# Optimization experiments

Hardware: AMD Instinct MI355X
Metric: run time of the kernel (lower is better)

The kernel has to match this reference:

```python
import jax, jax.numpy as jnp
import numpy as np

NEG_SLOPE = 0.2


def gat_layer(x, W, a_src, a_dst, b, src, dst, num_nodes, heads, out_c, concat):
    # Linear transform per head: [N, heads, out_c]
    h = (x @ W).reshape(num_nodes, heads, out_c)
    # Per-node attention logits for source/dest roles: [N, heads]
    e_src = jnp.einsum('nhc,hc->nh', h, a_src)
    e_dst = jnp.einsum('nhc,hc->nh', h, a_dst)
    # Edge-wise scores (gather), LeakyReLU: [E, heads]
    e = jax.nn.leaky_relu(e_src[src] + e_dst[dst], negative_slope=NEG_SLOPE)
    # Segment softmax over incoming edges of each destination node
    m = jax.ops.segment_max(e, dst, num_segments=num_nodes)
    ex = jnp.exp(e - m[dst])
    denom = jax.ops.segment_sum(ex, dst, num_segments=num_nodes)
    alpha = ex / denom[dst]                       # [E, heads]
    # Weighted scatter-aggregate of source messages: [N, heads, out_c]
    out = jax.ops.segment_sum(h[src] * alpha[:, :, None], dst, num_segments=num_nodes)
    if concat:
        out = out.reshape(num_nodes, heads * out_c)
    else:
        out = out.mean(axis=1)
    return out + b


def setup_inputs() -> dict:
    key = jax.random.key(0)
    ks = jax.random.split(key, 12)
    N, E = 50000, 800000
    in_c, out_c, heads = 128, 32, 4
    x = jax.random.normal(ks[0], (N, in_c), dtype=jnp.float32)
    edge_index = jax.random.randint(ks[1], (2, E), 0, N, dtype=jnp.int64)
    s1 = 1.0 / np.sqrt(in_c)
    W1 = jax.random.normal(ks[2], (in_c, heads * out_c), dtype=jnp.float32) * s1
    a_src1 = jax.random.normal(ks[3], (heads, out_c), dtype=jnp.float32) * 0.1
    a_dst1 = jax.random.normal(ks[4], (heads, out_c), dtype=jnp.float32) * 0.1
    b1 = jnp.zeros((heads * out_c,), dtype=jnp.float32)
    s2 = 1.0 / np.sqrt(heads * out_c)
    W2 = jax.random.normal(ks[5], (heads * out_c, out_c), dtype=jnp.float32) * s2
    a_src2 = jax.random.normal(ks[6], (1, out_c), dtype=jnp.float32) * 0.1
    a_dst2 = jax.random.normal(ks[7], (1, out_c), dtype=jnp.float32) * 0.1
    b2 = jnp.zeros((out_c,), dtype=jnp.float32)
    return {"x": x, "edge_index": edge_index, "W1": W1, "a_src1": a_src1,
            "a_dst1": a_dst1, "b1": b1, "W2": W2, "a_src2": a_src2,
            "a_dst2": a_dst2, "b2": b2}


def reference(x, edge_index, W1, a_src1, a_dst1, b1, W2, a_src2, a_dst2, b2):
    N = x.shape[0]
    heads, out_c = a_src1.shape
    # add_self_loops=True (PyG default)
    loops = jnp.arange(N, dtype=edge_index.dtype)
    src = jnp.concatenate([edge_index[0], loops])
    dst = jnp.concatenate([edge_index[1], loops])
    h1 = gat_layer(x, W1, a_src1, a_dst1, b1, src, dst, N, heads, out_c, concat=True)
    h1 = jax.nn.elu(h1)
    out = gat_layer(h1, W2, a_src2, a_dst2, b2, src, dst, N, 1, out_c, concat=False)
    return out
```

## Files before the change

### kernel.cpp

```cpp
#include <hip/hip_runtime.h>
#include <hip/hip_bf16.h>

#define LRELU_SLOPE 0.2f
#define NB_SHIFT 7
#define NBLK 512

typedef __attribute__((ext_vector_type(8))) short short8;
typedef __attribute__((ext_vector_type(4))) float float4v;

__device__ inline float b2f(unsigned short u) {
    union { unsigned int i; float f; } v; v.i = ((unsigned int)u) << 16; return v.f;
}
__device__ inline unsigned short f2b(float f) {
    union { float f; unsigned int i; } v; v.f = f;
    unsigned int x = v.i;
    unsigned int r = x + 0x7fffu + ((x >> 16) & 1u);
    return (unsigned short)(r >> 16);
}
__device__ inline float lrelu(float x) { return x > 0.f ? x : LRELU_SLOPE * x; }

__global__ __launch_bounds__(256) void gemm1_mfma_kernel(
        const float* __restrict__ x, const float* __restrict__ W1,
        const float* __restrict__ a_src, const float* __restrict__ a_dst,
        unsigned short* __restrict__ h1b, float* __restrict__ es,
        float* __restrict__ ed, int N,
        const int* __restrict__ dst, int E, int Etot, int nb, int chunk,
        int* __restrict__ cnt) {
    __shared__ unsigned short xs[64][136];
    __shared__ unsigned short wt[128][136];
    int tid = threadIdx.x;
    int n0 = blockIdx.x * 64;

    for (int i = tid; i < 128 * 128; i += 256) {
        int k = i >> 7, n = i & 127;
        wt[n][k] = f2b(W1[i]);
    }
    {
        int rows = N - n0; if (rows > 64) rows = 64;
        const float4* xv = (const float4*)(x + (size_t)n0 * 128);
        int lim = rows * 32;
        for (int i = tid; i < lim; i += 256) {
            float4 v = xv[i];
            int r = i >> 5, c4 = (i & 31) << 2;
            uint2 p;
            p.x = (unsigned int)f2b(v.x) | ((unsigned int)f2b(v.y) << 16);
            p.y = (unsigned int)f2b(v.z) | ((unsigned int)f2b(v.w) << 16);
            *(uint2*)&xs[r][c4] = p;
        }
    }
    __syncthreads();

    int wave = tid >> 6;
    int lane = tid & 63;
    int lrow = lane & 15;
    int quad = lane >> 4;

    short8 afr[4];
#pragma unroll
    for (int kc = 0; kc < 4; kc++)
        afr[kc] = *(const short8*)&xs[wave * 16 + lrow][kc * 32 + quad * 8];
    __syncthreads();

#pragma unroll
    for (int ct = 0; ct < 8; ct++) {
        float4v acc = {0.f, 0.f, 0.f, 0.f};
#pragma unroll
        for (int kc = 0; kc < 4; kc++) {
            short8 bfr = *(const short8*)&wt[ct * 16 + lrow][kc * 32 + quad * 8];
            acc = __builtin_amdgcn_mfma_f32_16x16x32_bf16(afr[kc], bfr, acc, 0, 0, 0);
        }
#pragma unroll
        for (int r = 0; r < 4; r++) {
            int lr = wave * 16 + quad * 4 + r;
            xs[lr][ct * 16 + lrow] = f2b(acc[r]);
        }
    }
    __syncthreads();

    {
        int rows = N - n0; if (rows > 64) rows = 64;
        int lim4 = rows * 16;
        for (int i = tid; i < lim4; i += 256) {
            int r = i >> 4, c8 = i & 15;
            *(uint4*)&h1b[(size_t)(n0 + r) * 128 + c8 * 8] =
                *(const uint4*)&xs[r][c8 * 8];
        }
    }

    int row = tid >> 2, h = tid & 3;
    int rg = n0 + row;
    if (rg < N) {
        const float* ap = a_src + h * 32;
        const float* bp = a_dst + h * 32;
        float s = 0.f, d = 0.f;
#pragma unroll
        for (int c2 = 0; c2 < 16; c2++) {
            unsigned int u = *(const unsigned int*)&xs[row][h * 32 + 2 * c2];
            float v0 = b2f((unsigned short)(u & 0xffffu));
            float v1 = b2f((unsigned short)(u >> 16));
            float2 a = *(const float2*)&ap[2 * c2];
            float2 b = *(const float2*)&bp[2 * c2];
            s += v0 * a.x + v1 * a.y;
            d += v0 * b.x + v1 * b.y;
        }
        es[rg * 4 + h] = s;
        ed[rg * 4 + h] = d;
    }

    int* histm = (int*)&wt[0][0];
    int blk = blockIdx.x;
    if (blk < NBLK)
        for (int i = tid; i < nb; i += 256) histm[i] = 0;
    __syncthreads();
    if (blk < NBLK) {
        int lo = blk * chunk;
        int hi = lo + chunk; if (hi > Etot) hi = Etot;
        for (int i = lo + tid; i < hi; i += 256) {
            int d = (i < E) ? dst[i] : (i - E);
            atomicAdd(&histm[d >> NB_SHIFT], 1);
        }
    }
    __syncthreads();
    if (blk < NBLK)
        for (int b = tid; b < nb; b += 256)
            cnt[b * NBLK + blk] = histm[b];
}

__global__ __launch_bounds__(1024) void scanA_kernel(int* cnt, int* bsum, int M) {
    __shared__ int tile[1024];
    int i = blockIdx.x * 1024 + threadIdx.x;
    int v = (i < M) ? cnt[i] : 0;
    tile[threadIdx.x] = v;
    __syncthreads();
    for (int off = 1; off < 1024; off <<= 1) {
        int t = (threadIdx.x >= (unsigned)off) ? tile[threadIdx.x - off] : 0;
        __syncthreads();
        tile[threadIdx.x] += t;
        __syncthreads();
    }
    int incl = tile[threadIdx.x];
    if (i < M) cnt[i] = incl - v;
    if (threadIdx.x == 1023) bsum[blockIdx.x] = incl;
}

__device__ inline void boff_scan(const int* __restrict__ bsum, int nbA,
                                 int* boffl, int tid) {
    int v = (tid < nbA) ? bsum[tid] : 0;
    boffl[tid] = v;
    __syncthreads();
    for (int off = 1; off < 256; off <<= 1) {
        int t = (tid >= off) ? boffl[tid - off] : 0;
        __syncthreads();
        boffl[tid] += t;
        __syncthreads();
    }
    int excl = boffl[tid] - v;
    __syncthreads();
    boffl[tid] = excl;
    __syncthreads();
}

__global__ __launch_bounds__(256) void partition_kernel(
        const int* __restrict__ src, const int* __restrict__ dst,
        int E, int Etot, int nb, int chunk, int nbA,
        const int* __restrict__ cnt, const int* __restrict__ bsum,
        unsigned int* __restrict__ bkt) {
    __shared__ int cur[512];
    __shared__ int boffl[256];
    int tid = threadIdx.x;
    boff_scan(bsum, nbA, boffl, tid);
    int blk = blockIdx.x;
    for (int b = tid; b < nb; b += 256) {
        int idx = b * NBLK + blk;
        cur[b] = cnt[idx] + boffl[idx >> 10];
    }
    __syncthreads();
    int lo = blk * chunk;
    int hi = lo + chunk; if (hi > Etot) hi = Etot;
    for (int i = lo + tid; i < hi; i += 256) {
        int s, d;
        if (i < E) { s = src[i]; d = dst[i]; }
        else       { s = d = i - E; }
        int pos = atomicAdd(&cur[d >> NB_SHIFT], 1);
        bkt[pos] = ((unsigned int)(d & 127) << 20) | (unsigned int)s;
    }
}

__global__ __launch_bounds__(256) void finalize_kernel(
        const unsigned int* __restrict__ bkt, const int* __restrict__ cnt,
        const int* __restrict__ bsum, int nb, int nbA,
        const float* __restrict__ es, const float* __restrict__ ed,
        int* __restrict__ ptr, int* __restrict__ csr_src,
        _Float16* __restrict__ w1h, int N, int Etot) {
    __shared__ int deg[128];
    __shared__ int scn[128];
    __shared__ int cur[128];
    __shared__ int boffl[256];
    int tid = threadIdx.x;
    boff_scan(bsum, nbA, boffl, tid);
    int b = blockIdx.x;
    int idx0 = b * NBLK;
    int base = cnt[idx0] + boffl[idx0 >> 10];
    int nextbase;
    if (b + 1 < nb) {
        int idx1 = (b + 1) * NBLK;
        nextbase = cnt[idx1] + boffl[idx1 >> 10];
    } else nextbase = Etot;
    int count = nextbase - base;
    int node0 = b << NB_SHIFT;
    int nodes = N - node0; if (nodes > 128) nodes = 128;

    if (tid < 128) deg[tid] = 0;
    __syncthreads();
    for (int i = tid; i < count; i += 256)
        atomicAdd(&deg[bkt[base + i] >> 20], 1);
    __syncthreads();
    int v = (tid < 128) ? deg[tid] : 0;
    if (tid < 128) scn[tid] = v;
    __syncthreads();
    for (int off = 1; off < 128; off <<= 1) {
        int t = (tid < 128 && tid >= (unsigned)off) ? scn[tid - off] : 0;
        __syncthreads();
        if (tid < 128) scn[tid] += t;
        __syncthreads();
    }
    if (tid < 128) {
        int excl = scn[tid] - v;
        cur[tid] = excl;
        if (tid < nodes) ptr[node0 + tid] = base + excl;
    }
    if (b == nb - 1 && tid == 0) ptr[N] = Etot;
    __syncthreads();
    for (int i = tid; i < count; i += 256) {
        unsigned int p = bkt[base + i];
        int dloc = p >> 20;
        int s = (int)(p & 0xFFFFFu);
        int pos = base + atomicAdd(&cur[dloc], 1);
        csr_src[pos] = s;
        float4 a = *(const float4*)&es[s * 4];
        float4 bb = *(const float4*)&ed[(node0 + dloc) * 4];
        union { _Float16 h[4]; uint2 u; } ww;
        ww.h[0] = (_Float16)__expf(lrelu(a.x + bb.x));
        ww.h[1] = (_Float16)__expf(lrelu(a.y + bb.y));
        ww.h[2] = (_Float16)__expf(lrelu(a.z + bb.z));
        ww.h[3] = (_Float16)__expf(lrelu(a.w + bb.w));
        *(uint2*)&w1h[(size_t)pos * 4] = ww.u;
    }
}

__global__ __launch_bounds__(256) void gemm2_mfma_kernel(
        const unsigned short* __restrict__ h1e, const float* __restrict__ W2,
        const float* __restrict__ a_src, const float* __restrict__ a_dst,
        unsigned short* __restrict__ h2b, float* __restrict__ es,
        float* __restrict__ ed, int N) {
    __shared__ unsigned short xs[64][136];
    __shared__ unsigned short wt[32][136];
    int tid = threadIdx.x;
    int n0 = blockIdx.x * 64;

    for (int i = tid; i < 128 * 32; i += 256) {
        int k = i >> 5, n = i & 31;
        wt[n][k] = f2b(W2[i]);
    }
    {
        const unsigned int* srcp = (const unsigned int*)(h1e + (size_t)n0 * 128);
        int rows = (N - n0) < 64 ? (N - n0) : 64;
        int maxu = rows * 64;
        for (int i = tid; i < 4096; i += 256) {
            unsigned int v = (i < maxu) ? srcp[i] : 0u;
            int r = i >> 6, cp = (i & 63) << 1;
            *(unsigned int*)&xs[r][cp] = v;
        }
    }
    __syncthreads();

    int wave = tid >> 6;
    int lane = tid & 63;
    int lrow = lane & 15;
    int quad = lane >> 4;

    short8 afr[4];
#pragma unroll
    for (int kc = 0; kc < 4; kc++)
        afr[kc] = *(const short8*)&xs[wave * 16 + lrow][kc * 32 + quad * 8];
    __syncthreads();

#pragma unroll
    for (int ct = 0; ct < 2; ct++) {
        float4v acc = {0.f, 0.f, 0.f, 0.f};
#pragma unroll
        for (int kc = 0; kc < 4; kc++) {
            short8 bfr = *(const short8*)&wt[ct * 16 + lrow][kc * 32 + quad * 8];
            acc = __builtin_amdgcn_mfma_f32_16x16x32_bf16(afr[kc], bfr, acc, 0, 0, 0);
        }
#pragma unroll
        for (int r = 0; r < 4; r++) {
            int lr = wave * 16 + quad * 4 + r;
            xs[lr][ct * 16 + lrow] = f2b(acc[r]);
        }
    }
    __syncthreads();

    {
        int rows = (N - n0) < 64 ? (N - n0) : 64;
        int lim4 = rows * 4;
        for (int i = tid; i < lim4; i += 256) {
            int r = i >> 2, c8 = i & 3;
            *(uint4*)&h2b[(size_t)(n0 + r) * 32 + c8 * 8] =
                *(const uint4*)&xs[r][c8 * 8];
        }
    }

    if (tid < 64) {
        int rg = n0 + tid;
        if (rg < N) {
            float s = 0.f, d = 0.f;
#pragma unroll
            for (int c2 = 0; c2 < 16; c2++) {
                unsigned int u = *(const unsigned int*)&xs[tid][2 * c2];
                float v0 = b2f((unsigned short)(u & 0xffffu));
                float v1 = b2f((unsigned short)(u >> 16));
                float2 a = *(const float2*)&a_src[2 * c2];
                float2 b = *(const float2*)&a_dst[2 * c2];
                s += v0 * a.x + v1 * a.y;
                d += v0 * b.x + v1 * b.y;
            }
            es[rg] = s;
            ed[rg] = d;
        }
    }
}

__global__ __launch_bounds__(256) void agg1_kernel(
        const uint4* __restrict__ h1v, const _Float16* __restrict__ w1h,
        const int* __restrict__ csr, const int* __restrict__ ptr,
        const float* __restrict__ b1, uint4* __restrict__ h1e_v, int N) {
    int tid = threadIdx.x;
    int n = blockIdx.x * 16 + (tid >> 4);
    if (n >= N) return;
    int cl = tid & 15;
    int h = cl >> 2;
    int start = ptr[n], end = ptr[n + 1];
    float a0 = 0.f, a1 = 0.f, a2 = 0.f, a3 = 0.f;
    float a4 = 0.f, a5 = 0.f, a6 = 0.f, a7 = 0.f, ws = 0.f;
    int i = start;
    for (; i + 4 <= end; i += 4) {
        int s[4]; float v[4]; uint4 g[4];
#pragma unroll
        for (int k = 0; k < 4; k++) s[k] = csr[i + k];
#pragma unroll
        for (int k = 0; k < 4; k++) v[k] = (float)w1h[(size_t)(i + k) * 4 + h];
#pragma unroll
        for (int k = 0; k < 4; k++) g[k] = h1v[(s[k] << 4) + cl];
#pragma unroll
        for (int k = 0; k < 4; k++) {
            a0 += v[k] * b2f((unsigned short)(g[k].x & 0xffffu));
            a1 += v[k] * b2f((unsigned short)(g[k].x >> 16));
            a2 += v[k] * b2f((unsigned short)(g[k].y & 0xffffu));
            a3 += v[k] * b2f((unsigned short)(g[k].y >> 16));
            a4 += v[k] * b2f((unsigned short)(g[k].z & 0xffffu));
            a5 += v[k] * b2f((unsigned short)(g[k].z >> 16));
            a6 += v[k] * b2f((unsigned short)(g[k].w & 0xffffu));
            a7 += v[k] * b2f((unsigned short)(g[k].w >> 16));
            ws += v[k];
        }
    }
    for (; i < end; i++) {
        int s = csr[i];
        float v = (float)w1h[(size_t)i * 4 + h];
        uint4 g = h1v[(s << 4) + cl];
        a0 += v * b2f((unsigned short)(g.x & 0xffffu));
        a1 += v * b2f((unsigned short)(g.x >> 16));
        a2 += v * b2f((unsigned short)(g.y & 0xffffu));
        a3 += v * b2f((unsigned short)(g.y >> 16));
        a4 += v * b2f((unsigned short)(g.z & 0xffffu));
        a5 += v * b2f((unsigned short)(g.z >> 16));
        a6 += v * b2f((unsigned short)(g.w & 0xffffu));
        a7 += v * b2f((unsigned short)(g.w >> 16));
        ws += v;
    }
    float r = 1.f / ws;
    float4 bb0 = ((const float4*)b1)[cl * 2];
    float4 bb1 = ((const float4*)b1)[cl * 2 + 1];
    float o0 = a0 * r + bb0.x;
    float o1 = a1 * r + bb0.y;
    float o2 = a2 * r + bb0.z;
    float o3 = a3 * r + bb0.w;
    float o4 = a4 * r + bb1.x;
    float o5 = a5 * r + bb1.y;
    float o6 = a6 * r + bb1.z;
    float o7 = a7 * r + bb1.w;
    o0 = o0 > 0.f ? o0 : __expf(o0) - 1.f;
    o1 = o1 > 0.f ? o1 : __expf(o1) - 1.f;
    o2 = o2 > 0.f ? o2 : __expf(o2) - 1.f;
    o3 = o3 > 0.f ? o3 : __expf(o3) - 1.f;
    o4 = o4 > 0.f ? o4 : __expf(o4) - 1.f;
    o5 = o5 > 0.f ? o5 : __expf(o5) - 1.f;
    o6 = o6 > 0.f ? o6 : __expf(o6) - 1.f;
    o7 = o7 > 0.f ? o7 : __expf(o7) - 1.f;
    uint4 outv;
    outv.x = (unsigned int)f2b(o0) | ((unsigned int)f2b(o1) << 16);
    outv.y = (unsigned int)f2b(o2) | ((unsigned int)f2b(o3) << 16);
    outv.z = (unsigned int)f2b(o4) | ((unsigned int)f2b(o5) << 16);
    outv.w = (unsigned int)f2b(o6) | ((unsigned int)f2b(o7) << 16);
    h1e_v[(n << 4) + cl] = outv;
}

__global__ __launch_bounds__(256) void agg2_kernel(
        const uint2* __restrict__ h2v, const float* __restrict__ es,
        const float* __restrict__ ed, const int* __restrict__ csr,
        const int* __restrict__ ptr, const float* __restrict__ b2,
        float* __restrict__ out, int N) {
    int tid = threadIdx.x;
    int n = blockIdx.x * 32 + (tid >> 3);
    if (n >= N) return;
    int cl = tid & 7;
    float edl = ed[n];
    int start = ptr[n], end = ptr[n + 1];
    float a0 = 0.f, a1 = 0.f, a2 = 0.f, a3 = 0.f, ws = 0.f;
    int i = start;
    for (; i + 8 <= end; i += 8) {
        int s[8]; float e[8]; uint2 g[8];
#pragma unroll
        for (int k = 0; k < 8; k++) s[k] = csr[i + k];
#pragma unroll
        for (int k = 0; k < 8; k++) e[k] = es[s[k]];
#pragma unroll
        for (int k = 0; k < 8; k++) g[k] = h2v[(s[k] << 3) + cl];
#pragma unroll
        for (int k = 0; k < 8; k++) {
            float v = __expf(lrelu(e[k] + edl));
            a0 += v * b2f((unsigned short)(g[k].x & 0xffffu));
            a1 += v * b2f((unsigned short)(g[k].x >> 16));
            a2 += v * b2f((unsigned short)(g[k].y & 0xffffu));
            a3 += v * b2f((unsigned short)(g[k].y >> 16));
            ws += v;
        }
    }
    for (; i < end; i++) {
        int s = csr[i];
        float v = __expf(lrelu(es[s] + edl));
        uint2 g = h2v[(s << 3) + cl];
        a0 += v * b2f((unsigned short)(g.x & 0xffffu));
        a1 += v * b2f((unsigned short)(g.x >> 16));
        a2 += v * b2f((unsigned short)(g.y & 0xffffu));
        a3 += v * b2f((unsigned short)(g.y >> 16));
        ws += v;
    }
    float r = 1.f / ws;
    float4 bb = ((const float4*)b2)[cl];
    float4 o;
    o.x = a0 * r + bb.x;
    o.y = a1 * r + bb.y;
    o.z = a2 * r + bb.z;
    o.w = a3 * r + bb.w;
    ((float4*)out)[(size_t)n * 8 + cl] = o;
}

extern "C" void kernel_launch(void* const* d_in, const int* in_sizes, int n_in,
                              void* d_out, int out_size, void* d_ws, size_t ws_size,
                              hipStream_t stream) {
    const float* x      = (const float*)d_in[0];
    const int*   ei     = (const int*)  d_in[1];
    const float* W1     = (const float*)d_in[2];
    const float* a_src1 = (const float*)d_in[3];
    const float* a_dst1 = (const float*)d_in[4];
    const float* b1     = (const float*)d_in[5];
    const float* W2     = (const float*)d_in[6];
    const float* a_src2 = (const float*)d_in[7];
    const float* a_dst2 = (const float*)d_in[8];
    const float* b2     = (const float*)d_in[9];
    float* outp = (float*)d_out;

    const int N = in_sizes[0] / 128;
    const int E = in_sizes[1] / 2;
    const int Etot = E + N;

    const int* src = ei;
    const int* dst = ei + E;

    const int nb    = (N + 127) >> 7;
    const int chunk = (Etot + NBLK - 1) / NBLK;
    const int M = nb * NBLK;
    const int nbA = (M + 1023) / 1024;

    char* w = (char*)d_ws;
    unsigned short* h1b = (unsigned short*)(w + 0);
    unsigned short* h1e = (unsigned short*)(w + 12800000);
    unsigned short* h2b = (unsigned short*)(w + 25600000);
    float* es1  = (float*)(w + 28800000);
    float* ed1  = (float*)(w + 29600000);
    float* es2  = (float*)(w + 30400000);
    float* ed2  = (float*)(w + 30600000);
    int*   ptr  = (int*)  (w + 30800000);
    int*   bsum = (int*)  (w + 31000064);
    int*   cnt  = (int*)  (w + 31001088);
    int*   csr_src = (int*)(w + 31801856);
    unsigned int* bkt = (unsigned int*)(w + 35201856);
    _Float16* w1h = (_Float16*)(w + 42001856);

    gemm1_mfma_kernel<<<(N + 63) / 64, 256, 0, stream>>>(x, W1, a_src1, a_dst1,
                                                         h1b, es1, ed1, N,
                                                         dst, E, Etot, nb, chunk,
                                                         cnt);

    scanA_kernel<<<nbA, 1024, 0, stream>>>(cnt, bsum, M);
    partition_kernel<<<NBLK, 256, 0, stream>>>(src, dst, E, Etot, nb, chunk, nbA,
                                               cnt, bsum, bkt);
    finalize_kernel<<<nb, 256, 0, stream>>>(bkt, cnt, bsum, nb, nbA, es1, ed1,
                                            ptr, csr_src, w1h, N, Etot);

    agg1_kernel<<<(N + 15) / 16, 256, 0, stream>>>((const uint4*)h1b, w1h,
                                                   csr_src, ptr, b1,
                                                   (uint4*)h1e, N);

    gemm2_mfma_kernel<<<(N + 63) / 64, 256, 0, stream>>>(h1e, W2, a_src2, a_dst2,
                                                         h2b, es2, ed2, N);
    agg2_kernel<<<(N + 31) / 32, 256, 0, stream>>>((const uint2*)h2b, es2, ed2,
                                                   csr_src, ptr, b2, outp, N);
}
```

Before: 198.9 us.

## Fuse layer-1 aggregation with layer-2 linear transform and attention logits

Merges the agg1 kernel and the gemm2 MFMA kernel into a single kernel. Each 16-node block keeps its ELU-activated bf16 layer-1 outputs in shared memory and multiplies them by W2 (converted to bf16 in LDS) with scalar FMAs. It then computes the layer-2 source and destination logits with lane shuffles. This removes the 12.8 MB h1e write and read round trip and one kernel launch. In exchange, every block reconverts all of W2 into LDS, and the matrix product now runs on scalar ALUs instead of MFMA.

```diff
diff --git a/kernel.cpp b/kernel.cpp
--- a/kernel.cpp
+++ b/kernel.cpp
@@ -248,99 +248,29 @@
     }
 }
 
-__global__ __launch_bounds__(256) void gemm2_mfma_kernel(
-        const unsigned short* __restrict__ h1e, const float* __restrict__ W2,
-        const float* __restrict__ a_src, const float* __restrict__ a_dst,
-        unsigned short* __restrict__ h2b, float* __restrict__ es,
-        float* __restrict__ ed, int N) {
-    __shared__ unsigned short xs[64][136];
-    __shared__ unsigned short wt[32][136];
-    int tid = threadIdx.x;
-    int n0 = blockIdx.x * 64;
-
-    for (int i = tid; i < 128 * 32; i += 256) {
-        int k = i >> 5, n = i & 31;
-        wt[n][k] = f2b(W2[i]);
-    }
-    {
-        const unsigned int* srcp = (const unsigned int*)(h1e + (size_t)n0 * 128);
-        int rows = (N - n0) < 64 ? (N - n0) : 64;
-        int maxu = rows * 64;
-        for (int i = tid; i < 4096; i += 256) {
-            unsigned int v = (i < maxu) ? srcp[i] : 0u;
-            int r = i >> 6, cp = (i & 63) << 1;
-            *(unsigned int*)&xs[r][cp] = v;
-        }
-    }
-    __syncthreads();
-
-    int wave = tid >> 6;
-    int lane = tid & 63;
-    int lrow = lane & 15;
-    int quad = lane >> 4;
-
-    short8 afr[4];
-#pragma unroll
-    for (int kc = 0; kc < 4; kc++)
-        afr[kc] = *(const short8*)&xs[wave * 16 + lrow][kc * 32 + quad * 8];
-    __syncthreads();
-
-#pragma unroll
-    for (int ct = 0; ct < 2; ct++) {
-        float4v acc = {0.f, 0.f, 0.f, 0.f};
-#pragma unroll
-        for (int kc = 0; kc < 4; kc++) {
-            short8 bfr = *(const short8*)&wt[ct * 16 + lrow][kc * 32 + quad * 8];
-            acc = __builtin_amdgcn_mfma_f32_16x16x32_bf16(afr[kc], bfr, acc, 0, 0, 0);
-        }
-#pragma unroll
-        for (int r = 0; r < 4; r++) {
-            int lr = wave * 16 + quad * 4 + r;
-            xs[lr][ct * 16 + lrow] = f2b(acc[r]);
-        }
-    }
-    __syncthreads();
-
-    {
-        int rows = (N - n0) < 64 ? (N - n0) : 64;
-        int lim4 = rows * 4;
-        for (int i = tid; i < lim4; i += 256) {
-            int r = i >> 2, c8 = i & 3;
-            *(uint4*)&h2b[(size_t)(n0 + r) * 32 + c8 * 8] =
-                *(const uint4*)&xs[r][c8 * 8];
-        }
-    }
-
-    if (tid < 64) {
-        int rg = n0 + tid;
-        if (rg < N) {
-            float s = 0.f, d = 0.f;
-#pragma unroll
-            for (int c2 = 0; c2 < 16; c2++) {
-                unsigned int u = *(const unsigned int*)&xs[tid][2 * c2];
-                float v0 = b2f((unsigned short)(u & 0xffffu));
-                float v1 = b2f((unsigned short)(u >> 16));
-                float2 a = *(const float2*)&a_src[2 * c2];
-                float2 b = *(const float2*)&a_dst[2 * c2];
-                s += v0 * a.x + v1 * a.y;
-                d += v0 * b.x + v1 * b.y;
-            }
-            es[rg] = s;
-            ed[rg] = d;
-        }
-    }
-}
-
-__global__ __launch_bounds__(256) void agg1_kernel(
+__global__ __launch_bounds__(256) void agg1_gemm2_kernel(
         const uint4* __restrict__ h1v, const _Float16* __restrict__ w1h,
         const int* __restrict__ csr, const int* __restrict__ ptr,
-        const float* __restrict__ b1, uint4* __restrict__ h1e_v, int N) {
+        const float* __restrict__ b1, const float* __restrict__ W2,
+        const float* __restrict__ a_src2, const float* __restrict__ a_dst2,
+        unsigned short* __restrict__ h2b, float* __restrict__ es2,
+        float* __restrict__ ed2, int N) {
+    __shared__ unsigned short hs[16][136];
+    __shared__ unsigned short w2l[128][36];
     int tid = threadIdx.x;
+
+    for (int i = tid; i < 4096; i += 256) {
+        int k = i >> 5, c = i & 31;
+        w2l[k][c] = f2b(W2[i]);
+    }
+
     int n = blockIdx.x * 16 + (tid >> 4);
-    if (n >= N) return;
+    int node = tid >> 4;
     int cl = tid & 15;
     int h = cl >> 2;
-    int start = ptr[n], end = ptr[n + 1];
+    bool act = (n < N);
+    int start = 0, end = 0;
+    if (act) { start = ptr[n]; end = ptr[n + 1]; }
     float a0 = 0.f, a1 = 0.f, a2 = 0.f, a3 = 0.f;
     float a4 = 0.f, a5 = 0.f, a6 = 0.f, a7 = 0.f, ws = 0.f;
     int i = start;
@@ -379,31 +309,64 @@
         a7 += v * b2f((unsigned short)(g.w >> 16));
         ws += v;
     }
-    float r = 1.f / ws;
-    float4 bb0 = ((const float4*)b1)[cl * 2];
-    float4 bb1 = ((const float4*)b1)[cl * 2 + 1];
-    float o0 = a0 * r + bb0.x;
-    float o1 = a1 * r + bb0.y;
-    float o2 = a2 * r + bb0.z;
-    float o3 = a3 * r + bb0.w;
-    float o4 = a4 * r + bb1.x;
-    float o5 = a5 * r + bb1.y;
-    float o6 = a6 * r + bb1.z;
-    float o7 = a7 * r + bb1.w;
-    o0 = o0 > 0.f ? o0 : __expf(o0) - 1.f;
-    o1 = o1 > 0.f ? o1 : __expf(o1) - 1.f;
-    o2 = o2 > 0.f ? o2 : __expf(o2) - 1.f;
-    o3 = o3 > 0.f ? o3 : __expf(o3) - 1.f;
-    o4 = o4 > 0.f ? o4 : __expf(o4) - 1.f;
-    o5 = o5 > 0.f ? o5 : __expf(o5) - 1.f;
-    o6 = o6 > 0.f ? o6 : __expf(o6) - 1.f;
-    o7 = o7 > 0.f ? o7 : __expf(o7) - 1.f;
-    uint4 outv;
-    outv.x = (unsigned int)f2b(o0) | ((unsigned int)f2b(o1) << 16);
-    outv.y = (unsigned int)f2b(o2) | ((unsigned int)f2b(o3) << 16);
-    outv.z = (unsigned int)f2b(o4) | ((unsigned int)f2b(o5) << 16);
-    outv.w = (unsigned int)f2b(o6) | ((unsigned int)f2b(o7) << 16);
-    h1e_v[(n << 4) + cl] = outv;
+    if (act) {
+        float r = 1.f / ws;
+        float4 bb0 = ((const float4*)b1)[cl * 2];
+        float4 bb1 = ((const float4*)b1)[cl * 2 + 1];
+        float o0 = a0 * r + bb0.x;
+        float o1 = a1 * r + bb0.y;
+        float o2 = a2 * r + bb0.z;
+        float o3 = a3 * r + bb0.w;
+        float o4 = a4 * r + bb1.x;
+        float o5 = a5 * r + bb1.y;
+        float o6 = a6 * r + bb1.z;
+        float o7 = a7 * r + bb1.w;
+        o0 = o0 > 0.f ? o0 : __expf(o0) - 1.f;
+        o1 = o1 > 0.f ? o1 : __expf(o1) - 1.f;
+        o2 = o2 > 0.f ? o2 : __expf(o2) - 1.f;
+        o3 = o3 > 0.f ? o3 : __expf(o3) - 1.f;
+        o4 = o4 > 0.f ? o4 : __expf(o4) - 1.f;
+        o5 = o5 > 0.f ? o5 : __expf(o5) - 1.f;
+        o6 = o6 > 0.f ? o6 : __expf(o6) - 1.f;
+        o7 = o7 > 0.f ? o7 : __expf(o7) - 1.f;
+        uint4 outv;
+        outv.x = (unsigned int)f2b(o0) | ((unsigned int)f2b(o1) << 16);
+        outv.y = (unsigned int)f2b(o2) | ((unsigned int)f2b(o3) << 16);
+        outv.z = (unsigned int)f2b(o4) | ((unsigned int)f2b(o5) << 16);
+        outv.w = (unsigned int)f2b(o6) | ((unsigned int)f2b(o7) << 16);
+        *(uint4*)&hs[node][cl * 8] = outv;
+    }
+    __syncthreads();
+
+    if (act) {
+        int c2 = cl * 2;
+        float o0 = 0.f, o1 = 0.f;
+#pragma unroll 4
+        for (int k = 0; k < 128; k += 2) {
+            unsigned int hu = *(const unsigned int*)&hs[node][k];
+            float h0 = b2f((unsigned short)(hu & 0xffffu));
+            float h1 = b2f((unsigned short)(hu >> 16));
+            unsigned int w0 = *(const unsigned int*)&w2l[k][c2];
+            unsigned int w1 = *(const unsigned int*)&w2l[k + 1][c2];
+            o0 += h0 * b2f((unsigned short)(w0 & 0xffffu));
+            o1 += h0 * b2f((unsigned short)(w0 >> 16));
+            o0 += h1 * b2f((unsigned short)(w1 & 0xffffu));
+            o1 += h1 * b2f((unsigned short)(w1 >> 16));
+        }
+        unsigned short q0 = f2b(o0), q1 = f2b(o1);
+        *(unsigned int*)&h2b[(size_t)n * 32 + c2] =
+            (unsigned int)q0 | ((unsigned int)q1 << 16);
+        float vq0 = b2f(q0), vq1 = b2f(q1);
+        float2 as = *(const float2*)&a_src2[c2];
+        float2 ad = *(const float2*)&a_dst2[c2];
+        float s = vq0 * as.x + vq1 * as.y;
+        float d = vq0 * ad.x + vq1 * ad.y;
+        s += __shfl_xor(s, 1);  d += __shfl_xor(d, 1);
+        s += __shfl_xor(s, 2);  d += __shfl_xor(d, 2);
+        s += __shfl_xor(s, 4);  d += __shfl_xor(d, 4);
+        s += __shfl_xor(s, 8);  d += __shfl_xor(d, 8);
+        if (cl == 0) { es2[n] = s; ed2[n] = d; }
+    }
 }
 
 __global__ __launch_bounds__(256) void agg2_kernel(
@@ -486,7 +449,6 @@
 
     char* w = (char*)d_ws;
     unsigned short* h1b = (unsigned short*)(w + 0);
-    unsigned short* h1e = (unsigned short*)(w + 12800000);
     unsigned short* h2b = (unsigned short*)(w + 25600000);
     float* es1  = (float*)(w + 28800000);
     float* ed1  = (float*)(w + 29600000);
@@ -510,12 +472,11 @@
     finalize_kernel<<<nb, 256, 0, stream>>>(bkt, cnt, bsum, nb, nbA, es1, ed1,
                                             ptr, csr_src, w1h, N, Etot);
 
-    agg1_kernel<<<(N + 15) / 16, 256, 0, stream>>>((const uint4*)h1b, w1h,
-                                                   csr_src, ptr, b1,
-                                                   (uint4*)h1e, N);
-
-    gemm2_mfma_kernel<<<(N + 63) / 64, 256, 0, stream>>>(h1e, W2, a_src2, a_dst2,
+    agg1_gemm2_kernel<<<(N + 15) / 16, 256, 0, stream>>>((const uint4*)h1b, w1h,
+                                                         csr_src, ptr, b1, W2,
+                                                         a_src2, a_dst2,
                                                          h2b, es2, ed2, N);
+
     agg2_kernel<<<(N + 31) / 32, 256, 0, stream>>>((const uint2*)h2b, es2, ed2,
                                                    csr_src, ptr, b2, outp, N);
 }
```

Result: no change. 198.0 us (-0.5%).
